# Optimization experiments

Measured on AMD Instinct MI355X. Metric: run time of the kernel, lower is better.

## Reference

```python
import jax, jax.numpy as jnp
import numpy as np

B, S, D, H = 2, 2048, 1024, 16
DK = D // H

def setup_inputs() -> dict:
    key = jax.random.key(0)
    ks = jax.random.split(key, 8)
    scale = 1.0 / np.sqrt(D)
    return {
        "q": jax.random.normal(ks[0], (B, S, D), jnp.float32),
        "k": jax.random.normal(ks[1], (B, S, D), jnp.float32),
        "v": jax.random.normal(ks[2], (B, S, D), jnp.float32),
        "reaches": jax.random.uniform(ks[3], (B, S), jnp.float32),
        "Wq": jax.random.normal(ks[4], (D, D), jnp.float32) * scale,
        "Wk": jax.random.normal(ks[5], (D, D), jnp.float32) * scale,
        "Wv": jax.random.normal(ks[6], (D, D), jnp.float32) * scale,
        "Wo": jax.random.normal(ks[7], (D, D), jnp.float32) * scale,
    }

def _split_heads(x):
    # [B,S,D] -> [B,H,S,DK]
    return x.reshape(B, S, H, DK).transpose(0, 2, 1, 3)

def reference(q, k, v, reaches, Wq, Wk, Wv, Wo):
    # torch Linear: y = x @ W.T
    qh = _split_heads(q @ Wq.T)
    kh = _split_heads(k @ Wk.T)
    vh = _split_heads(v @ Wv.T)
    scores = jnp.einsum("bhqd,bhkd->bhqk", qh, kh) / jnp.sqrt(jnp.float32(DK))
    scores = jax.nn.softmax(scores, axis=-1)
    # post-softmax reach weighting along key axis
    scores = scores * reaches[:, None, None, :]
    # diagonal suppression: scores - scores*0.999999*eye
    scores = scores * (1.0 - 0.999999 * jnp.eye(S, dtype=scores.dtype))
    # inverted combine
    out = vh - jnp.einsum("bhqk,bhkd->bhqd", scores, vh)
    # per-position contribution rescale
    rs = reaches.sum(axis=-1, keepdims=True)
    contrib = (rs - reaches) / (rs + 1e-9) * (1.0 - reaches) * 100.0  # [B,S]
    out = out * contrib[:, None, :, None]
    concat = out.transpose(0, 2, 1, 3).reshape(B, S, D)
    return concat @ Wo.T
```

## Files before the change

kernel.cpp:

```cpp
#include <hip/hip_runtime.h>
#include <hip/hip_bf16.h>

typedef __attribute__((ext_vector_type(8))) short short8;
typedef __attribute__((ext_vector_type(4))) float f32x4;
typedef __attribute__((ext_vector_type(16))) float f32x16;
typedef unsigned short us;

#define B_ 2
#define S_ 2048
#define D_ 1024
#define H_ 16
#define DK_ 64
#define QSCALE 0.1803368867f

__device__ __forceinline__ us f2bf(float f) {
  union { float f; unsigned u; } x; x.f = f;
  unsigned r = x.u + 0x7FFFu + ((x.u >> 16) & 1u);
  return (us)(r >> 16);
}
__device__ __forceinline__ float bf2f(us h) {
  union { unsigned u; float f; } x; x.u = ((unsigned)h) << 16;
  return x.f;
}
__device__ __forceinline__ us f2bf_hw(float f) {
  __hip_bfloat16 h = __float2bfloat16(f);
  return *reinterpret_cast<us*>(&h);
}

__device__ __forceinline__ void gload16(const void* g, void* l) {
  __builtin_amdgcn_global_load_lds((const __attribute__((address_space(1))) void*)g,
                                   (__attribute__((address_space(3))) void*)l, 16, 0, 0);
}

__global__ __launch_bounds__(256) void cvt_all(const float* __restrict__ q,
                                               const float* __restrict__ k,
                                               const float* __restrict__ v,
                                               const float* __restrict__ Wq,
                                               const float* __restrict__ Wk,
                                               const float* __restrict__ Wv,
                                               const float* __restrict__ Wo,
                                               us* __restrict__ oq, us* __restrict__ ok,
                                               us* __restrict__ ov, us* __restrict__ oWq,
                                               us* __restrict__ oWk, us* __restrict__ oWv,
                                               us* __restrict__ oWo) {
  int bid = blockIdx.x;
  const float* in; us* out; int off;
  if (bid < 12288) {
    int t = bid >> 12;
    in = (t == 0) ? q : (t == 1) ? k : v;
    out = (t == 0) ? oq : (t == 1) ? ok : ov;
    off = (bid & 4095) * 1024;
  } else {
    int t = (bid - 12288) >> 10;
    in = (t == 0) ? Wq : (t == 1) ? Wk : (t == 2) ? Wv : Wo;
    out = (t == 0) ? oWq : (t == 1) ? oWk : (t == 2) ? oWv : oWo;
    off = ((bid - 12288) & 1023) * 1024;
  }
  int i = off + threadIdx.x * 4;
  float4 val = *reinterpret_cast<const float4*>(in + i);
  ushort4 o;
  o.x = f2bf(val.x); o.y = f2bf(val.y); o.z = f2bf(val.z); o.w = f2bf(val.w);
  *reinterpret_cast<ushort4*>(out + i) = o;
}

__global__ __launch_bounds__(256) void rs_kernel(const float* __restrict__ reaches,
                                                 float* __restrict__ rs) {
  int b = blockIdx.x, t = threadIdx.x;
  float s = 0.f;
  for (int i = t; i < S_; i += 256) s += reaches[b * S_ + i];
  for (int o = 32; o > 0; o >>= 1) s += __shfl_down(s, o, 64);
  __shared__ float tmp[4];
  if ((t & 63) == 0) tmp[t >> 6] = s;
  __syncthreads();
  if (t == 0) rs[b] = tmp[0] + tmp[1] + tmp[2] + tmp[3];
}

__device__ __forceinline__ void gemm_core_hs(const us* __restrict__ A, const us* __restrict__ Bt,
                                             us* __restrict__ outH, float oscale) {
  __shared__ __align__(16) us lA[128 * 32];
  __shared__ __align__(16) us lB[128 * 32];
  const int tid = threadIdx.x;
  const int bm = blockIdx.x >> 3, bn = blockIdx.x & 7;
  const int w = tid >> 6, lane = tid & 63;
  const int wr = (w >> 1) * 64, wc = (w & 1) * 64;
  const int lr = lane & 15, lg = lane >> 4;

  f32x4 acc[4][4];
#pragma unroll
  for (int i = 0; i < 4; ++i)
#pragma unroll
    for (int j = 0; j < 4; ++j) acc[i][j] = (f32x4){0.f, 0.f, 0.f, 0.f};

  const int crow = lane >> 2, ce8 = (lane & 3) * 8;
  const us* A0 = A + (size_t)(bm * 128 + w * 32 + crow) * 1024 + ce8;
  const us* A1 = A0 + (size_t)16 * 1024;
  const us* B0 = Bt + (size_t)(bn * 128 + w * 32 + crow) * 1024 + ce8;
  const us* B1 = B0 + (size_t)16 * 1024;
  us* lA0 = &lA[(w * 2) * 512]; us* lA1 = lA0 + 512;
  us* lB0 = &lB[(w * 2) * 512]; us* lB1 = lB0 + 512;

  for (int kt = 0; kt < 1024; kt += 32) {
    gload16(A0 + kt, lA0);
    gload16(A1 + kt, lA1);
    gload16(B0 + kt, lB0);
    gload16(B1 + kt, lB1);
    __syncthreads();
    short8 af[4], bfr[4];
#pragma unroll
    for (int i = 0; i < 4; ++i)
      af[i] = *reinterpret_cast<const short8*>(&lA[(wr + i * 16 + lr) * 32 + lg * 8]);
#pragma unroll
    for (int j = 0; j < 4; ++j)
      bfr[j] = *reinterpret_cast<const short8*>(&lB[(wc + j * 16 + lr) * 32 + lg * 8]);
#pragma unroll
    for (int i = 0; i < 4; ++i)
#pragma unroll
      for (int j = 0; j < 4; ++j)
        acc[i][j] = __builtin_amdgcn_mfma_f32_16x16x32_bf16(af[i], bfr[j], acc[i][j], 0, 0, 0);
    __syncthreads();
  }
#pragma unroll
  for (int i = 0; i < 4; ++i)
#pragma unroll
    for (int j = 0; j < 4; ++j)
#pragma unroll
      for (int ii = 0; ii < 4; ++ii) {
        int r = bm * 128 + wr + i * 16 + lg * 4 + ii;
        int c = bn * 128 + wc + j * 16 + lr;
        float v = acc[i][j][ii] * oscale;
        int b = r >> 11, s = r & (S_ - 1), h = c >> 6, dk = c & 63;
        outH[(((size_t)(b * H_ + h) * S_ + s) * DK_) + dk] = f2bf(v);
      }
}

__global__ __launch_bounds__(256) void proj_gemm(const us* __restrict__ q_bf,
                                                 const us* __restrict__ k_bf,
                                                 const us* __restrict__ v_bf,
                                                 const us* __restrict__ Wq_bf,
                                                 const us* __restrict__ Wk_bf,
                                                 const us* __restrict__ Wv_bf,
                                                 us* __restrict__ Qh, us* __restrict__ Kh,
                                                 us* __restrict__ Vh) {
  if (blockIdx.y == 0) gemm_core_hs(q_bf, Wq_bf, Qh, QSCALE);
  else if (blockIdx.y == 1) gemm_core_hs(k_bf, Wk_bf, Kh, 1.0f);
  else gemm_core_hs(v_bf, Wv_bf, Vh, 1.0f);
}

__global__ __launch_bounds__(256) void wo_gemm(const us* __restrict__ A,
                                               const us* __restrict__ Bt,
                                               float* __restrict__ outF) {
  __shared__ __align__(16) us lA[128 * 32];
  __shared__ __align__(16) us lB[64 * 32];
  const int tid = threadIdx.x;
  const int bm = blockIdx.x >> 4, bn = blockIdx.x & 15;
  const int w = tid >> 6, lane = tid & 63;
  const int lr = lane & 15, lg = lane >> 4;

  f32x4 acc[2][4];
#pragma unroll
  for (int i = 0; i < 2; ++i)
#pragma unroll
    for (int j = 0; j < 4; ++j) acc[i][j] = (f32x4){0.f, 0.f, 0.f, 0.f};

  const int crow = lane >> 2, ce8 = (lane & 3) * 8;
  const us* A0 = A + (size_t)(bm * 128 + w * 32 + crow) * 1024 + ce8;
  const us* A1 = A0 + (size_t)16 * 1024;
  const us* B0 = Bt + (size_t)(bn * 64 + w * 16 + crow) * 1024 + ce8;
  us* lA0 = &lA[w * 1024]; us* lA1 = lA0 + 512;
  us* lB0 = &lB[w * 512];

  for (int kt = 0; kt < 1024; kt += 32) {
    gload16(A0 + kt, lA0);
    gload16(A1 + kt, lA1);
    gload16(B0 + kt, lB0);
    __syncthreads();
    short8 af[2], bfr[4];
#pragma unroll
    for (int i = 0; i < 2; ++i)
      af[i] = *reinterpret_cast<const short8*>(&lA[(w * 32 + i * 16 + lr) * 32 + lg * 8]);
#pragma unroll
    for (int j = 0; j < 4; ++j)
      bfr[j] = *reinterpret_cast<const short8*>(&lB[(j * 16 + lr) * 32 + lg * 8]);
#pragma unroll
    for (int i = 0; i < 2; ++i)
#pragma unroll
      for (int j = 0; j < 4; ++j)
        acc[i][j] = __builtin_amdgcn_mfma_f32_16x16x32_bf16(af[i], bfr[j], acc[i][j], 0, 0, 0);
    __syncthreads();
  }
#pragma unroll
  for (int i = 0; i < 2; ++i)
#pragma unroll
    for (int j = 0; j < 4; ++j)
#pragma unroll
      for (int ii = 0; ii < 4; ++ii) {
        int r = bm * 128 + w * 32 + i * 16 + lg * 4 + ii;
        int c = bn * 64 + j * 16 + lr;
        outF[(size_t)r * 1024 + c] = acc[i][j][ii];
      }
}

__global__ __launch_bounds__(256) void transp_kernel(const us* __restrict__ Vh,
                                                     const float* __restrict__ reaches,
                                                     us* __restrict__ VhTw) {
  __shared__ us t[64 * 68];
  const int bh = blockIdx.x >> 5, st = blockIdx.x & 31;
  const int b = bh >> 4;
  const size_t base = (size_t)bh * S_ * DK_;
  const int r = threadIdx.x >> 3, e8 = (threadIdx.x & 7) * 8;
#pragma unroll
  for (int h2 = 0; h2 < 2; ++h2) {
    int row = r + h2 * 32;
    *reinterpret_cast<short8*>(&t[row * 68 + e8]) =
        *reinterpret_cast<const short8*>(&Vh[base + (size_t)(st * 64 + row) * DK_ + e8]);
  }
  __syncthreads();
#pragma unroll
  for (int h2 = 0; h2 < 2; ++h2) {
    int dk = (threadIdx.x >> 3) + h2 * 32;
    int sc = (threadIdx.x & 7) * 8;
    short8 v;
#pragma unroll
    for (int j = 0; j < 8; ++j) {
      float rw = reaches[b * S_ + st * 64 + sc + j];
      v[j] = (short)f2bf_hw(bf2f(t[(sc + j) * 68 + dk]) * rw);
    }
    *reinterpret_cast<short8*>(&VhTw[base + (size_t)dk * S_ + st * 64 + sc]) = v;
  }
}

__global__ __launch_bounds__(256, 2) void attn_kernel(const us* __restrict__ Qh,
                                                      const us* __restrict__ Kh,
                                                      const us* __restrict__ Vh,
                                                      const us* __restrict__ VhTw,
                                                      const float* __restrict__ reaches,
                                                      const float* __restrict__ rsum,
                                                      us* __restrict__ concat) {
  __shared__ __align__(16) us lK2[2][64 * 64];
  __shared__ __align__(16) us vT2[2][64 * 64];
  __shared__ __align__(16) us pw[128 * 72];
  __shared__ float diagP[128];

  const int tid = threadIdx.x;
  const int bid = ((blockIdx.x & 7) << 6) | (blockIdx.x >> 3);
  const int qt = bid & 15;
  const int bh = bid >> 4;
  const int b = bh >> 4, h = bh & 15;
  const size_t base = (size_t)bh * S_ * DK_;

  const int w = tid >> 6, lane = tid & 63;
  const int l31 = lane & 31, hh = lane >> 5, l7 = lane & 7;
  const int h4 = hh * 4;
  const int r2 = tid >> 3, e8 = (tid & 7) * 8;
  const int diagkt = qt * 2 + (w >> 1);

  short8 aq[4];
  {
    const us* qp = &Qh[base + (size_t)(qt * 128 + w * 32 + l31) * DK_ + hh * 8];
#pragma unroll
    for (int dk = 0; dk < 4; ++dk)
      aq[dk] = *reinterpret_cast<const short8*>(qp + dk * 16);
  }

  int rdK[2][4], rdV[2][4], rdP[4];
#pragma unroll
  for (int c = 0; c < 2; ++c)
#pragma unroll
    for (int dk = 0; dk < 4; ++dk) {
      rdK[c][dk] = (c * 32 + l31) * 64 + (((dk * 2 + hh) ^ l7) << 3);
      rdV[c][dk] = rdK[c][dk];
    }
#pragma unroll
  for (int ks = 0; ks < 4; ++ks) rdP[ks] = (w * 32 + l31) * 72 + ks * 16 + hh * 8;
  const int pwW = (w * 32 + h4) * 72 + l31;
  const int wslot = ((tid & 7) ^ (r2 & 7)) << 3;
  const int wK0 = r2 * 64 + wslot, wK1 = (r2 + 32) * 64 + wslot;

  short8 pk0, pk1, pv0, pv1;
  pk0 = *reinterpret_cast<const short8*>(&Kh[base + (size_t)r2 * DK_ + e8]);
  pk1 = *reinterpret_cast<const short8*>(&Kh[base + (size_t)(r2 + 32) * DK_ + e8]);
  pv0 = *reinterpret_cast<const short8*>(&VhTw[base + (size_t)r2 * S_ + e8]);
  pv1 = *reinterpret_cast<const short8*>(&VhTw[base + (size_t)(r2 + 32) * S_ + e8]);
  *reinterpret_cast<short8*>(&lK2[0][wK0]) = pk0;
  *reinterpret_cast<short8*>(&lK2[0][wK1]) = pk1;
  *reinterpret_cast<short8*>(&vT2[0][wK0]) = pv0;
  *reinterpret_cast<short8*>(&vT2[0][wK1]) = pv1;
  __syncthreads();

  f32x16 oacc[2];
  float lacc[16];
#pragma unroll
  for (int c = 0; c < 2; ++c)
#pragma unroll
    for (int r = 0; r < 16; ++r) oacc[c][r] = 0.f;
#pragma unroll
  for (int r = 0; r < 16; ++r) lacc[r] = 0.f;

  for (int kt = 0; kt < 32; ++kt) {
    const int cur = kt & 1;
    if (kt < 31) {
      int nt = kt + 1;
      pk0 = *reinterpret_cast<const short8*>(&Kh[base + (size_t)(nt * 64 + r2) * DK_ + e8]);
      pk1 = *reinterpret_cast<const short8*>(&Kh[base + (size_t)(nt * 64 + r2 + 32) * DK_ + e8]);
      pv0 = *reinterpret_cast<const short8*>(&VhTw[base + (size_t)r2 * S_ + nt * 64 + e8]);
      pv1 = *reinterpret_cast<const short8*>(&VhTw[base + (size_t)(r2 + 32) * S_ + nt * 64 + e8]);
    }

    f32x16 sf0, sf1;
#pragma unroll
    for (int r = 0; r < 16; ++r) { sf0[r] = 0.f; sf1[r] = 0.f; }
    __builtin_amdgcn_s_setprio(1);
#pragma unroll
    for (int dk = 0; dk < 4; ++dk) {
      short8 b0 = *reinterpret_cast<const short8*>(&lK2[cur][rdK[0][dk]]);
      sf0 = __builtin_amdgcn_mfma_f32_32x32x16_bf16(aq[dk], b0, sf0, 0, 0, 0);
      short8 b1 = *reinterpret_cast<const short8*>(&lK2[cur][rdK[1][dk]]);
      sf1 = __builtin_amdgcn_mfma_f32_32x32x16_bf16(aq[dk], b1, sf1, 0, 0, 0);
    }
    __builtin_amdgcn_s_setprio(0);

#pragma unroll
    for (int r = 0; r < 16; ++r) {
      const int rowc = (r & 3) + 8 * (r >> 2);
      float e0 = __builtin_amdgcn_exp2f(sf0[r]);
      float e1 = __builtin_amdgcn_exp2f(sf1[r]);
      lacc[r] += e0 + e1;
      pw[pwW + rowc * 72] = f2bf_hw(e0);
      pw[pwW + rowc * 72 + 32] = f2bf_hw(e1);
    }
    if (kt == diagkt) {
#pragma unroll
      for (int r = 0; r < 16; ++r) {
        const int myrow = (r & 3) + 8 * (r >> 2) + h4;
        float e = __builtin_amdgcn_exp2f((w & 1) ? sf1[r] : sf0[r]);
        if (l31 == myrow) diagP[w * 32 + myrow] = e;
      }
    }

    short8 pa[4];
#pragma unroll
    for (int ks = 0; ks < 4; ++ks)
      pa[ks] = *reinterpret_cast<const short8*>(&pw[rdP[ks]]);
    __builtin_amdgcn_s_setprio(1);
#pragma unroll
    for (int dc = 0; dc < 2; ++dc)
#pragma unroll
      for (int ks = 0; ks < 4; ++ks) {
        short8 bv = *reinterpret_cast<const short8*>(&vT2[cur][rdV[dc][ks]]);
        oacc[dc] = __builtin_amdgcn_mfma_f32_32x32x16_bf16(pa[ks], bv, oacc[dc], 0, 0, 0);
      }
    __builtin_amdgcn_s_setprio(0);

    if (kt < 31) {
      const int nx = cur ^ 1;
      *reinterpret_cast<short8*>(&lK2[nx][wK0]) = pk0;
      *reinterpret_cast<short8*>(&lK2[nx][wK1]) = pk1;
      *reinterpret_cast<short8*>(&vT2[nx][wK0]) = pv0;
      *reinterpret_cast<short8*>(&vT2[nx][wK1]) = pv1;
    }
    __syncthreads();
  }

#pragma unroll
  for (int o = 1; o <= 16; o <<= 1)
#pragma unroll
    for (int r = 0; r < 16; ++r) lacc[r] += __shfl_xor(lacc[r], o, 64);

  const float rb = rsum[b];
#pragma unroll
  for (int r = 0; r < 16; ++r) {
    const int q = w * 32 + (r & 3) + 8 * (r >> 2) + h4;
    const int qg = qt * 128 + q;
    const float rq = reaches[b * S_ + qg];
    const float contrib = (rb - rq) / (rb + 1e-9f) * (1.f - rq) * 100.f;
    const float corr = 0.999999f * diagP[q] * rq;
    const float linv = 1.0f / lacc[r];
#pragma unroll
    for (int dc = 0; dc < 2; ++dc) {
      int d = dc * 32 + l31;
      float vhv = bf2f(Vh[base + (size_t)qg * DK_ + d]);
      float pv = (oacc[dc][r] - corr * vhv) * linv;
      float o = (vhv - pv) * contrib;
      concat[((size_t)(b * S_ + qg)) * D_ + h * 64 + d] = f2bf(o);
    }
  }
}

extern "C" void kernel_launch(void* const* d_in, const int* in_sizes, int n_in,
                              void* d_out, int out_size, void* d_ws, size_t ws_size,
                              hipStream_t stream) {
  const float* q = (const float*)d_in[0];
  const float* k = (const float*)d_in[1];
  const float* v = (const float*)d_in[2];
  const float* reaches = (const float*)d_in[3];
  const float* Wq = (const float*)d_in[4];
  const float* Wk = (const float*)d_in[5];
  const float* Wv = (const float*)d_in[6];
  const float* Wo = (const float*)d_in[7];

  const size_t NQKV = (size_t)B_ * S_ * D_;
  const size_t NW = (size_t)D_ * D_;

  us* q_bf = (us*)d_ws;
  us* k_bf = q_bf + NQKV;
  us* v_bf = k_bf + NQKV;
  us* Wq_bf = v_bf + NQKV;
  us* Wk_bf = Wq_bf + NW;
  us* Wv_bf = Wk_bf + NW;
  us* Wo_bf = Wv_bf + NW;
  us* Qh = Wo_bf + NW;
  us* Kh = Qh + NQKV;
  us* Vh = Kh + NQKV;
  us* concat = Vh + NQKV;
  float* rs = (float*)(concat + NQKV);
  us* VhTw = q_bf;

  cvt_all<<<16384, 256, 0, stream>>>(q, k, v, Wq, Wk, Wv, Wo,
                                     q_bf, k_bf, v_bf, Wq_bf, Wk_bf, Wv_bf, Wo_bf);
  rs_kernel<<<B_, 256, 0, stream>>>(reaches, rs);

  proj_gemm<<<dim3(256, 3), 256, 0, stream>>>(q_bf, k_bf, v_bf, Wq_bf, Wk_bf, Wv_bf, Qh, Kh, Vh);
  transp_kernel<<<B_ * H_ * (S_ / 64), 256, 0, stream>>>(Vh, reaches, VhTw);

  attn_kernel<<<B_ * H_ * (S_ / 128), 256, 0, stream>>>(Qh, Kh, Vh, VhTw, reaches, rs, concat);

  wo_gemm<<<512, 256, 0, stream>>>(concat, Wo_bf, (float*)d_out);
}
```

Baseline: 141.3 us.

## Compute transposed scores and repack P in registers instead of LDS round-trip

New measurement: 133.1 us. 1.06x faster.

```diff
diff --git a/kernel.cpp b/kernel.cpp
--- a/kernel.cpp
+++ b/kernel.cpp
@@ -25,6 +25,11 @@
 __device__ __forceinline__ us f2bf_hw(float f) {
   __hip_bfloat16 h = __float2bfloat16(f);
   return *reinterpret_cast<us*>(&h);
+}
+__device__ __forceinline__ unsigned cvtpk(float lo, float hi) {
+  unsigned r;
+  asm("v_cvt_pk_bf16_f32 %0, %1, %2" : "=v"(r) : "v"(lo), "v"(hi));
+  return r;
 }
 
 __device__ __forceinline__ void gload16(const void* g, void* l) {
@@ -238,8 +243,8 @@
                                                       us* __restrict__ concat) {
   __shared__ __align__(16) us lK2[2][64 * 64];
   __shared__ __align__(16) us vT2[2][64 * 64];
-  __shared__ __align__(16) us pw[128 * 72];
   __shared__ float diagP[128];
+  __shared__ float lsum[128];
 
   const int tid = threadIdx.x;
   const int bid = ((blockIdx.x & 7) << 6) | (blockIdx.x >> 3);
@@ -262,17 +267,12 @@
       aq[dk] = *reinterpret_cast<const short8*>(qp + dk * 16);
   }
 
-  int rdK[2][4], rdV[2][4], rdP[4];
+  int rdK[2][4];
 #pragma unroll
   for (int c = 0; c < 2; ++c)
 #pragma unroll
-    for (int dk = 0; dk < 4; ++dk) {
+    for (int dk = 0; dk < 4; ++dk)
       rdK[c][dk] = (c * 32 + l31) * 64 + (((dk * 2 + hh) ^ l7) << 3);
-      rdV[c][dk] = rdK[c][dk];
-    }
-#pragma unroll
-  for (int ks = 0; ks < 4; ++ks) rdP[ks] = (w * 32 + l31) * 72 + ks * 16 + hh * 8;
-  const int pwW = (w * 32 + h4) * 72 + l31;
   const int wslot = ((tid & 7) ^ (r2 & 7)) << 3;
   const int wK0 = r2 * 64 + wslot, wK1 = (r2 + 32) * 64 + wslot;
 
@@ -288,13 +288,11 @@
   __syncthreads();
 
   f32x16 oacc[2];
-  float lacc[16];
+  float lacc = 0.f;
 #pragma unroll
   for (int c = 0; c < 2; ++c)
 #pragma unroll
     for (int r = 0; r < 16; ++r) oacc[c][r] = 0.f;
-#pragma unroll
-  for (int r = 0; r < 16; ++r) lacc[r] = 0.f;
 
   for (int kt = 0; kt < 32; ++kt) {
     const int cur = kt & 1;
@@ -306,47 +304,64 @@
       pv1 = *reinterpret_cast<const short8*>(&VhTw[base + (size_t)(r2 + 32) * S_ + nt * 64 + e8]);
     }
 
-    f32x16 sf0, sf1;
-#pragma unroll
-    for (int r = 0; r < 16; ++r) { sf0[r] = 0.f; sf1[r] = 0.f; }
+    f32x16 st0, st1;
+#pragma unroll
+    for (int r = 0; r < 16; ++r) { st0[r] = 0.f; st1[r] = 0.f; }
     __builtin_amdgcn_s_setprio(1);
 #pragma unroll
     for (int dk = 0; dk < 4; ++dk) {
-      short8 b0 = *reinterpret_cast<const short8*>(&lK2[cur][rdK[0][dk]]);
-      sf0 = __builtin_amdgcn_mfma_f32_32x32x16_bf16(aq[dk], b0, sf0, 0, 0, 0);
-      short8 b1 = *reinterpret_cast<const short8*>(&lK2[cur][rdK[1][dk]]);
-      sf1 = __builtin_amdgcn_mfma_f32_32x32x16_bf16(aq[dk], b1, sf1, 0, 0, 0);
+      short8 k0 = *reinterpret_cast<const short8*>(&lK2[cur][rdK[0][dk]]);
+      st0 = __builtin_amdgcn_mfma_f32_32x32x16_bf16(k0, aq[dk], st0, 0, 0, 0);
+      short8 k1 = *reinterpret_cast<const short8*>(&lK2[cur][rdK[1][dk]]);
+      st1 = __builtin_amdgcn_mfma_f32_32x32x16_bf16(k1, aq[dk], st1, 0, 0, 0);
     }
     __builtin_amdgcn_s_setprio(0);
 
+    float e0[16], e1[16];
 #pragma unroll
     for (int r = 0; r < 16; ++r) {
-      const int rowc = (r & 3) + 8 * (r >> 2);
-      float e0 = __builtin_amdgcn_exp2f(sf0[r]);
-      float e1 = __builtin_amdgcn_exp2f(sf1[r]);
-      lacc[r] += e0 + e1;
-      pw[pwW + rowc * 72] = f2bf_hw(e0);
-      pw[pwW + rowc * 72 + 32] = f2bf_hw(e1);
+      e0[r] = __builtin_amdgcn_exp2f(st0[r]);
+      e1[r] = __builtin_amdgcn_exp2f(st1[r]);
+      lacc += e0[r] + e1[r];
     }
     if (kt == diagkt) {
 #pragma unroll
       for (int r = 0; r < 16; ++r) {
-        const int myrow = (r & 3) + 8 * (r >> 2) + h4;
-        float e = __builtin_amdgcn_exp2f((w & 1) ? sf1[r] : sf0[r]);
-        if (l31 == myrow) diagP[w * 32 + myrow] = e;
+        int kk = (r & 3) + 8 * (r >> 2) + 4 * hh;
+        float ev = (w & 1) ? e1[r] : e0[r];
+        if (kk == l31) diagP[w * 32 + l31] = ev;
       }
     }
 
     short8 pa[4];
 #pragma unroll
-    for (int ks = 0; ks < 4; ++ks)
-      pa[ks] = *reinterpret_cast<const short8*>(&pw[rdP[ks]]);
+    for (int ks = 0; ks < 4; ++ks) {
+      const int ro = (ks & 1) * 8;
+      unsigned d0, s0, d1, s1;
+      if (ks < 2) {
+        d0 = cvtpk(e0[ro + 0], e0[ro + 1]);
+        s0 = cvtpk(e0[ro + 4], e0[ro + 5]);
+        d1 = cvtpk(e0[ro + 2], e0[ro + 3]);
+        s1 = cvtpk(e0[ro + 6], e0[ro + 7]);
+      } else {
+        d0 = cvtpk(e1[ro + 0], e1[ro + 1]);
+        s0 = cvtpk(e1[ro + 4], e1[ro + 5]);
+        d1 = cvtpk(e1[ro + 2], e1[ro + 3]);
+        s1 = cvtpk(e1[ro + 6], e1[ro + 7]);
+      }
+      asm("v_permlane32_swap_b32 %0, %1" : "+v"(d0), "+v"(s0));
+      asm("v_permlane32_swap_b32 %0, %1" : "+v"(d1), "+v"(s1));
+      union { unsigned u[4]; short8 v; } pk;
+      pk.u[0] = d0; pk.u[1] = d1; pk.u[2] = s0; pk.u[3] = s1;
+      pa[ks] = pk.v;
+    }
+
     __builtin_amdgcn_s_setprio(1);
 #pragma unroll
     for (int dc = 0; dc < 2; ++dc)
 #pragma unroll
       for (int ks = 0; ks < 4; ++ks) {
-        short8 bv = *reinterpret_cast<const short8*>(&vT2[cur][rdV[dc][ks]]);
+        short8 bv = *reinterpret_cast<const short8*>(&vT2[cur][rdK[dc][ks]]);
         oacc[dc] = __builtin_amdgcn_mfma_f32_32x32x16_bf16(pa[ks], bv, oacc[dc], 0, 0, 0);
       }
     __builtin_amdgcn_s_setprio(0);
@@ -361,10 +376,9 @@
     __syncthreads();
   }
 
-#pragma unroll
-  for (int o = 1; o <= 16; o <<= 1)
-#pragma unroll
-    for (int r = 0; r < 16; ++r) lacc[r] += __shfl_xor(lacc[r], o, 64);
+  lacc += __shfl_xor(lacc, 32, 64);
+  if (hh == 0) lsum[w * 32 + l31] = lacc;
+  __syncthreads();
 
   const float rb = rsum[b];
 #pragma unroll
@@ -374,7 +388,7 @@
     const float rq = reaches[b * S_ + qg];
     const float contrib = (rb - rq) / (rb + 1e-9f) * (1.f - rq) * 100.f;
     const float corr = 0.999999f * diagP[q] * rq;
-    const float linv = 1.0f / lacc[r];
+    const float linv = 1.0f / lsum[q];
 #pragma unroll
     for (int dc = 0; dc < 2; ++dc) {
       int d = dc * 32 + l31;
```
